# Kernel optimization log

Hardware: AMD Instinct MI355X
Metric: run time of the kernel (lower is better)

The kernel has to match this reference:

```python
import jax, jax.numpy as jnp
import numpy as np

B, S, Nv, D, DF, H = 8, 1024, 768, 512, 2048, 8
DH = D // H
EPS = 1e-5


def _layernorm(x, g, b):
    mu = jnp.mean(x, axis=-1, keepdims=True)
    var = jnp.mean((x - mu) ** 2, axis=-1, keepdims=True)
    return (x - mu) * jax.lax.rsqrt(var + EPS) * g + b


def _mha(x, Wq, Wk, Wv, Wo):
    b, s, d = x.shape
    q = (x @ Wq).reshape(b, s, H, DH)
    k = (x @ Wk).reshape(b, s, H, DH)
    v = (x @ Wv).reshape(b, s, H, DH)
    scores = jnp.einsum('bqhd,bkhd->bhqk', q, k) / np.sqrt(DH).astype(np.float32)
    a = jax.nn.softmax(scores, axis=-1)
    o = jnp.einsum('bhqk,bkhd->bqhd', a, v).reshape(b, s, d)
    return o @ Wo


def setup_inputs() -> dict:
    key = jax.random.key(0)
    ks = jax.random.split(key, 20)
    sc = 1.0 / np.sqrt(D)
    scf = 1.0 / np.sqrt(DF)
    n = lambda k, shp, s: (jax.random.normal(k, shp, jnp.float32) * s)
    return {
        'x': n(ks[0], (B, S, D), 1.0),
        'idx_emb_1': jax.random.randint(ks[1], (B, Nv), 0, Nv, dtype=jnp.int64) if jax.config.jax_enable_x64 else jax.random.randint(ks[1], (B, Nv), 0, Nv).astype(jnp.int32),
        'idx_pro_1': jax.random.randint(ks[2], (B, Nv), 0, Nv).astype(jnp.int32),
        'N': Nv,
        'Wq1': n(ks[3], (D, D), sc), 'Wk1': n(ks[4], (D, D), sc),
        'Wv1': n(ks[5], (D, D), sc), 'Wo1': n(ks[6], (D, D), sc),
        'Wq2': n(ks[7], (D, D), sc), 'Wk2': n(ks[8], (D, D), sc),
        'Wv2': n(ks[9], (D, D), sc), 'Wo2': n(ks[10], (D, D), sc),
        'w_conv1': n(ks[11], (D, DF), sc), 'b_conv1': jnp.zeros((DF,), jnp.float32),
        'w_conv2': n(ks[12], (DF, D), scf), 'b_conv2': jnp.zeros((D,), jnp.float32),
        'g1': jnp.ones((D,), jnp.float32), 'beta1': jnp.zeros((D,), jnp.float32),
        'g2': jnp.ones((D,), jnp.float32), 'beta2': jnp.zeros((D,), jnp.float32),
    }


def reference(x, idx_emb_1, idx_pro_1, N,
              Wq1, Wk1, Wv1, Wo1, Wq2, Wk2, Wv2, Wo2,
              w_conv1, b_conv1, w_conv2, b_conv2, g1, beta1, g2, beta2):
    # batched gather-reorder of first N tokens; rest pass through
    x_l1 = x.at[:, :N].set(jnp.take_along_axis(x[:, :N], idx_emb_1[:, :, None].astype(jnp.int32), axis=1))
    attn1 = _mha(x_l1, Wq1, Wk1, Wv1, Wo1)
    attn2 = jnp.flip(_mha(jnp.flip(x_l1, axis=1), Wq2, Wk2, Wv2, Wo2), axis=1)
    new_x1 = attn1 + attn2
    x_l2 = new_x1.at[:, :N].set(jnp.take_along_axis(new_x1[:, :N], idx_pro_1[:, :, None].astype(jnp.int32), axis=1))
    x = _layernorm(x + x_l2, g1, beta1)
    # kernel-size-1 Conv1d FFN == pointwise linear (dropout=0, eval mode)
    y = jnp.maximum(x @ w_conv1 + b_conv1, 0.0)
    y = y @ w_conv2 + b_conv2
    out = _layernorm(x + y, g2, beta2)
    return (out, attn1, attn2)
```

## Files before the change

kernel.cpp:

```cpp
#include <hip/hip_runtime.h>
#include <hip/hip_bf16.h>
#include <stdint.h>

#define B_ 8
#define S_ 1024
#define NV_ 768
#define D_ 512
#define DF_ 2048
#define H_ 8
#define DH_ 64
#define BS_ (B_*S_)
#define BSD_ ((size_t)B_*S_*D_)
#define QKLD 2048

typedef __bf16 bf16x8 __attribute__((ext_vector_type(8)));
typedef float f32x4 __attribute__((ext_vector_type(4)));
typedef float f32x16 __attribute__((ext_vector_type(16)));
typedef __hip_bfloat16 bf16;

__device__ __forceinline__ void async_copy16(const void* g, void* l) {
  __builtin_amdgcn_global_load_lds((const __attribute__((address_space(1))) void*)g,
                                   (__attribute__((address_space(3))) void*)l, 16, 0, 0);
}

__device__ __forceinline__ void stage_tile(const bf16* __restrict__ g, int gRow0, long ldg,
                                           int gCol0, bf16* lds, int rows, int tid) {
  const int totalBytes = rows << 7;
  for (int off = tid * 16; off < totalBytes; off += 4096) {
    const int r = off >> 7;
    const int c = off & 127;
    const int srcByte = c ^ ((r & 7) << 4);
    const bf16* gp = g + (long)(gRow0 + r) * ldg + gCol0 + (srcByte >> 1);
    async_copy16(gp, (char*)lds + off);
  }
}
__device__ __forceinline__ bf16x8 lds_frag(const bf16* base, int row, int kElem) {
  const int byte = (row << 7) + ((kElem << 1) ^ ((row & 7) << 4));
  return *(const bf16x8*)((const char*)base + byte);
}

__device__ __forceinline__ int fswz(int row) {
  return ((((row >> 3) & 3) << 1) | (row & 1)) << 4;
}

#define SCH_BIAS 1064872540.f
template<int BASE>
__device__ __forceinline__ bf16x8 pexp_frag(const f32x16& s) {
  union { unsigned u[4]; bf16x8 b; } r;
#pragma unroll
  for (int e = 0; e < 4; e++) {
    const int i0 = (int)fmaf(s[BASE + 2 * e], 8388608.f, SCH_BIAS);
    const int i1 = (int)fmaf(s[BASE + 2 * e + 1], 8388608.f, SCH_BIAS);
    r.u[e] = __builtin_amdgcn_perm((unsigned)i1, (unsigned)i0, 0x07060302u);
  }
  return r.b;
}

__device__ __forceinline__ bf16x8 ones_frag() {
  union { ushort u[8]; bf16x8 b; } r;
#pragma unroll
  for (int e = 0; e < 8; e++) r.u[e] = 0x3F80;
  return r.b;
}

__device__ __forceinline__ f32x16 zero16() {
  f32x16 z;
#pragma unroll
  for (int i = 0; i < 16; i++) z[i] = 0.f;
  return z;
}

struct WPanel { const float* src; bf16* dst; int srcLd, dstLd; float scale; };
struct WP16 { WPanel p[16]; };
__global__ __launch_bounds__(256) void wtrans16_kernel(WP16 ws) {
  __shared__ float tile[32][33];
  const WPanel pa = ws.p[blockIdx.z];
  const int tx = threadIdx.x, ty = threadIdx.y;
  const int n0 = blockIdx.x * 32, k0 = blockIdx.y * 32;
#pragma unroll
  for (int i = 0; i < 4; i++)
    tile[ty + i * 8][tx] = pa.src[(long)(k0 + ty + i * 8) * pa.srcLd + n0 + tx];
  __syncthreads();
#pragma unroll
  for (int i = 0; i < 4; i++)
    pa.dst[(long)(n0 + ty + i * 8) * pa.dstLd + k0 + tx] =
        __float2bfloat16(tile[tx][ty + i * 8] * pa.scale);
}

__global__ __launch_bounds__(256) void gather_cvt_kernel(const float* __restrict__ x,
                                                         const int* __restrict__ idx,
                                                         const int* __restrict__ Np,
                                                         bf16* __restrict__ out) {
  const int N = *Np;
  const int row = blockIdx.x * 2 + (threadIdx.x >> 7);
  const int t = threadIdx.x & 127;
  const int b = row >> 10, s = row & 1023;
  const int src = (s < N) ? idx[b * NV_ + s] : s;
  const float4 v = *(const float4*)(x + ((long)b * S_ + src) * D_ + t * 4);
  ushort4 u;
  u.x = (ushort)__bfloat16_as_ushort(__float2bfloat16(v.x));
  u.y = (ushort)__bfloat16_as_ushort(__float2bfloat16(v.y));
  u.z = (ushort)__bfloat16_as_ushort(__float2bfloat16(v.z));
  u.w = (ushort)__bfloat16_as_ushort(__float2bfloat16(v.w));
  *(ushort4*)(out + (long)row * D_ + t * 4) = u;
}

template<int BM, int BN, int MR, int NR, int OUTF, int BIAS, int RELU, int QKV>
__global__ __launch_bounds__(256) void gemm_bt(const bf16* __restrict__ A, long lda, long sAz,
                                               const bf16* __restrict__ Bt, long sBz,
                                               const float* __restrict__ bias,
                                               void* __restrict__ C, long ldc, long sCz,
                                               int K, bf16* __restrict__ vtbOut) {
  constexpr int WC = BN / (NR * 16);
  constexpr int WR = BM / (MR * 16);
  static_assert(WR * WC == 4, "4 waves");
  __shared__ bf16 As[BM * 64];
  __shared__ bf16 Bs[BN * 64];
  const int tid = threadIdx.x;
  const int lane = tid & 63, wave = tid >> 6;
  const int wr = wave / WC, wc = wave % WC;
  const int g = lane >> 4, lr = lane & 15;
  const int m0 = blockIdx.x * BM, n0 = blockIdx.y * BN;
  const int z = blockIdx.z;
  A += (long)z * sAz;
  Bt += (long)z * sBz;

  f32x4 acc[MR][NR];
#pragma unroll
  for (int m = 0; m < MR; m++)
#pragma unroll
    for (int n = 0; n < NR; n++) acc[m][n] = (f32x4){0.f, 0.f, 0.f, 0.f};

  for (int kt = 0; kt < K; kt += 64) {
    stage_tile(A, m0, lda, kt, As, BM, tid);
    stage_tile(Bt, n0, K, kt, Bs, BN, tid);
    __syncthreads();
#pragma unroll
    for (int ks = 0; ks < 64; ks += 32) {
      const int kk = ks + g * 8;
      bf16x8 aF[MR], bF[NR];
#pragma unroll
      for (int m = 0; m < MR; m++) aF[m] = lds_frag(As, wr * (MR * 16) + m * 16 + lr, kk);
#pragma unroll
      for (int n = 0; n < NR; n++) bF[n] = lds_frag(Bs, wc * (NR * 16) + n * 16 + lr, kk);
#pragma unroll
      for (int m = 0; m < MR; m++)
#pragma unroll
        for (int n = 0; n < NR; n++)
          acc[m][n] = __builtin_amdgcn_mfma_f32_16x16x32_bf16(aF[m], bF[n], acc[m][n], 0, 0, 0);
    }
    __syncthreads();
  }

#pragma unroll
  for (int m = 0; m < MR; m++) {
#pragma unroll
    for (int n = 0; n < NR; n++) {
      const int row = m0 + wr * (MR * 16) + m * 16 + g * 4;
      const int col = n0 + wc * (NR * 16) + n * 16 + lr;
      if (QKV) {
        const int set = (col >= 1536) ? 1 : 0;
        const int c1 = col - set * 1536;
        if (c1 < 1024) {
          bf16* cp = (bf16*)C + (long)row * QKLD + set * 1024 + c1;
#pragma unroll
          for (int r = 0; r < 4; r++) cp[(long)r * QKLD] = __float2bfloat16(acc[m][n][r]);
        } else {
          const int d = c1 - 1024;
          const int zz = set * 64 + ((row >> 10) << 3) + (d >> 6);
          const int s = row & 1023;
          const int sp = (s & ~12) | ((s & 4) << 1) | ((s & 8) >> 1);
          ushort4 pk;
          pk.x = (ushort)__bfloat16_as_ushort(__float2bfloat16(acc[m][n][0]));
          pk.y = (ushort)__bfloat16_as_ushort(__float2bfloat16(acc[m][n][1]));
          pk.z = (ushort)__bfloat16_as_ushort(__float2bfloat16(acc[m][n][2]));
          pk.w = (ushort)__bfloat16_as_ushort(__float2bfloat16(acc[m][n][3]));
          *(ushort4*)(vtbOut + (((long)(zz * 64 + (d & 63))) << 10) + sp) = pk;
        }
      } else {
        const float bv = BIAS ? bias[col] : 0.f;
#pragma unroll
        for (int r = 0; r < 4; r++) {
          float v = acc[m][n][r] + bv;
          if (RELU) v = fmaxf(v, 0.f);
          if (OUTF) ((float*)C)[(long)z * sCz + (long)(row + r) * ldc + col] = v;
          else ((bf16*)C)[(long)z * sCz + (long)(row + r) * ldc + col] = __float2bfloat16(v);
        }
      }
    }
  }
}

__global__ __launch_bounds__(256, 4) void flash_kernel(bf16* __restrict__ qk,
                                                       const bf16* __restrict__ vtb) {
  __shared__ char lds[32768];
  const int tid = threadIdx.x;
  const int lane = tid & 63, warp = tid >> 6;
  const int qlo = lane & 31, hi = lane >> 5;

  const int bid = (int)blockIdx.x;
  const int swz = (bid & 7) * 128 + (bid >> 3);
  const int qt = swz & 7;
  const int sbh = swz >> 3;
  const int set = sbh >> 6;
  const int b = (sbh >> 3) & 7, h = sbh & 7;

  bf16* Qp = qk + (long)b * S_ * QKLD + set * 1024 + h * DH_;
  const bf16* Kp = Qp + 512;
  const bf16* Vp = vtb + (long)sbh * DH_ * S_;

  const int r0 = tid >> 3;
  const int cbyt = (tid & 7) << 4;
  const int sb = cbyt ^ fswz(r0);
  char* const ld0 = lds + tid * 16;

  {
    const bf16* qS = Qp + (long)(qt * 128 + r0) * QKLD + (sb >> 1);
    async_copy16(qS, ld0);
    async_copy16(qS + 32 * QKLD, ld0 + 4096);
    async_copy16(qS + 64 * QKLD, ld0 + 8192);
    async_copy16(qS + 96 * QKLD, ld0 + 12288);
  }
  const bf16* kS = Kp + (long)r0 * QKLD + (sb >> 1);
  const bf16* vS = Vp + (long)r0 * S_ + (sb >> 1);
  async_copy16(kS, ld0 + 16384);
  async_copy16(kS + 32 * QKLD, ld0 + 16384 + 4096);
  async_copy16(vS, ld0 + 16384 + 8192);
  async_copy16(vS + 32 * S_, ld0 + 16384 + 12288);
  __syncthreads();

  const int qrow = warp * 32 + qlo;
  const int qrb = (qrow << 7) | fswz(qrow);
  bf16x8 qFh[4];
#pragma unroll
  for (int d4 = 0; d4 < 4; d4++)
    qFh[d4] = *(const bf16x8*)(lds + (qrb ^ (d4 * 32 + hi * 16)));
  __syncthreads();

  kS += 64 * QKLD; vS += 64;
  async_copy16(kS, ld0);
  async_copy16(kS + 32 * QKLD, ld0 + 4096);
  async_copy16(vS, ld0 + 8192);
  async_copy16(vS + 32 * S_, ld0 + 12288);

  f32x16 oAcc0 = zero16(), oAcc1 = zero16(), sAcc = zero16();
  const bf16x8 onesF = ones_frag();
  const int rb = (qlo << 7) | fswz(qlo);

  for (int t = 0; t < 16; t++) {
    const int bb = ((t & 1) ^ 1) << 14;
    const int kbase = bb + rb;
    const int vbase = bb + 8192 + rb;

    f32x16 s0 = zero16(), s1 = zero16();
    __builtin_amdgcn_s_setprio(1);
#pragma unroll
    for (int d4 = 0; d4 < 4; d4++) {
      const int kc2 = d4 * 32 + hi * 16;
      const bf16x8 kf0 = *(const bf16x8*)(lds + (kbase ^ kc2));
      const bf16x8 kf1 = *(const bf16x8*)(lds + ((kbase + 4096) ^ kc2));
      s0 = __builtin_amdgcn_mfma_f32_32x32x16_bf16(kf0, qFh[d4], s0, 0, 0, 0);
      s1 = __builtin_amdgcn_mfma_f32_32x32x16_bf16(kf1, qFh[d4], s1, 0, 0, 0);
    }
    __builtin_amdgcn_s_setprio(0);

    __builtin_amdgcn_s_setprio(1);
    {
      const bf16x8 pa0 = pexp_frag<0>(s0);
      oAcc0 = __builtin_amdgcn_mfma_f32_32x32x16_bf16(pa0, *(const bf16x8*)(lds + ((vbase) ^ (hi * 16))), oAcc0, 0, 0, 0);
      oAcc1 = __builtin_amdgcn_mfma_f32_32x32x16_bf16(pa0, *(const bf16x8*)(lds + ((vbase + 4096) ^ (hi * 16))), oAcc1, 0, 0, 0);
      sAcc = __builtin_amdgcn_mfma_f32_32x32x16_bf16(pa0, onesF, sAcc, 0, 0, 0);
      const bf16x8 pa1 = pexp_frag<8>(s0);
      oAcc0 = __builtin_amdgcn_mfma_f32_32x32x16_bf16(pa1, *(const bf16x8*)(lds + ((vbase) ^ (32 + hi * 16))), oAcc0, 0, 0, 0);
      oAcc1 = __builtin_amdgcn_mfma_f32_32x32x16_bf16(pa1, *(const bf16x8*)(lds + ((vbase + 4096) ^ (32 + hi * 16))), oAcc1, 0, 0, 0);
      sAcc = __builtin_amdgcn_mfma_f32_32x32x16_bf16(pa1, onesF, sAcc, 0, 0, 0);
      const bf16x8 pa2 = pexp_frag<0>(s1);
      oAcc0 = __builtin_amdgcn_mfma_f32_32x32x16_bf16(pa2, *(const bf16x8*)(lds + ((vbase) ^ (64 + hi * 16))), oAcc0, 0, 0, 0);
      oAcc1 = __builtin_amdgcn_mfma_f32_32x32x16_bf16(pa2, *(const bf16x8*)(lds + ((vbase + 4096) ^ (64 + hi * 16))), oAcc1, 0, 0, 0);
      sAcc = __builtin_amdgcn_mfma_f32_32x32x16_bf16(pa2, onesF, sAcc, 0, 0, 0);
      const bf16x8 pa3 = pexp_frag<8>(s1);
      oAcc0 = __builtin_amdgcn_mfma_f32_32x32x16_bf16(pa3, *(const bf16x8*)(lds + ((vbase) ^ (96 + hi * 16))), oAcc0, 0, 0, 0);
      oAcc1 = __builtin_amdgcn_mfma_f32_32x32x16_bf16(pa3, *(const bf16x8*)(lds + ((vbase + 4096) ^ (96 + hi * 16))), oAcc1, 0, 0, 0);
      sAcc = __builtin_amdgcn_mfma_f32_32x32x16_bf16(pa3, onesF, sAcc, 0, 0, 0);
    }
    __builtin_amdgcn_s_setprio(0);

    __syncthreads();
    if (t + 2 < 16) {
      kS += 64 * QKLD; vS += 64;
      char* dst = ld0 + bb;
      async_copy16(kS, dst);
      async_copy16(kS + 32 * QKLD, dst + 4096);
      async_copy16(vS, dst + 8192);
      async_copy16(vS + 32 * S_, dst + 12288);
    }
  }

#pragma unroll
  for (int r = 0; r < 16; r++) {
    const int q = (r & 3) + 8 * (r >> 2) + 4 * hi;
    const float linv = 1.f / sAcc[r];
    bf16* op = Qp + (long)(qt * 128 + warp * 32 + q) * QKLD;
    op[qlo] = __float2bfloat16(oAcc0[r] * linv);
    op[32 + qlo] = __float2bfloat16(oAcc1[r] * linv);
  }
}

__global__ __launch_bounds__(256) void fuse1_kernel(const float* __restrict__ x,
                                                    const float* __restrict__ a1,
                                                    const float* __restrict__ a2,
                                                    const int* __restrict__ idx,
                                                    const int* __restrict__ Np,
                                                    const float* __restrict__ gw,
                                                    const float* __restrict__ bw,
                                                    bf16* __restrict__ xlnB) {
  const int N = *Np;
  const int row = blockIdx.x * 4 + (threadIdx.x >> 6);
  const int lane = threadIdx.x & 63;
  const int b = row >> 10, s = row & 1023;
  const int j = (s < N) ? idx[b * NV_ + s] : s;
  const float* xp = x + (long)row * D_ + lane * 8;
  const float* p1 = a1 + ((long)b * S_ + j) * D_ + lane * 8;
  const float* p2 = a2 + ((long)b * S_ + j) * D_ + lane * 8;
  float v[8];
  float sum = 0.f;
#pragma unroll
  for (int q = 0; q < 2; q++) {
    const float4 t = ((const float4*)xp)[q];
    const float4 u = ((const float4*)p1)[q];
    const float4 w = ((const float4*)p2)[q];
    v[q * 4 + 0] = t.x + u.x + w.x; v[q * 4 + 1] = t.y + u.y + w.y;
    v[q * 4 + 2] = t.z + u.z + w.z; v[q * 4 + 3] = t.w + u.w + w.w;
  }
#pragma unroll
  for (int i = 0; i < 8; i++) sum += v[i];
#pragma unroll
  for (int o = 1; o < 64; o <<= 1) sum += __shfl_xor(sum, o, 64);
  const float mu = sum * (1.f / D_);
  float var = 0.f;
#pragma unroll
  for (int i = 0; i < 8; i++) { const float t = v[i] - mu; var += t * t; }
#pragma unroll
  for (int o = 1; o < 64; o <<= 1) var += __shfl_xor(var, o, 64);
  const float rs = rsqrtf(var * (1.f / D_) + 1e-5f);
#pragma unroll
  for (int i = 0; i < 8; i++) {
    const int d = lane * 8 + i;
    xlnB[(long)row * D_ + d] = __float2bfloat16((v[i] - mu) * rs * gw[d] + bw[d]);
  }
}

__global__ __launch_bounds__(256) void fuse2_kernel(const bf16* __restrict__ xlnB,
                                                    const bf16* __restrict__ ybf,
                                                    const float* __restrict__ gw,
                                                    const float* __restrict__ bw,
                                                    float* __restrict__ out) {
  const int row = blockIdx.x * 4 + (threadIdx.x >> 6);
  const int lane = threadIdx.x & 63;
  const bf16* xp = xlnB + (long)row * D_ + lane * 8;
  const bf16* yp = ybf + (long)row * D_ + lane * 8;
  float v[8];
  float sum = 0.f;
#pragma unroll
  for (int i = 0; i < 8; i++) {
    v[i] = __bfloat162float(xp[i]) + __bfloat162float(yp[i]);
    sum += v[i];
  }
#pragma unroll
  for (int o = 1; o < 64; o <<= 1) sum += __shfl_xor(sum, o, 64);
  const float mu = sum * (1.f / D_);
  float var = 0.f;
#pragma unroll
  for (int i = 0; i < 8; i++) { const float t = v[i] - mu; var += t * t; }
#pragma unroll
  for (int o = 1; o < 64; o <<= 1) var += __shfl_xor(var, o, 64);
  const float rs = rsqrtf(var * (1.f / D_) + 1e-5f);
#pragma unroll
  for (int i = 0; i < 8; i++) {
    const int d = lane * 8 + i;
    out[(long)row * D_ + d] = (v[i] - mu) * rs * gw[d] + bw[d];
  }
}

extern "C" void kernel_launch(void* const* d_in, const int* in_sizes, int n_in,
                              void* d_out, int out_size, void* d_ws, size_t ws_size,
                              hipStream_t stream) {
  const float* x   = (const float*)d_in[0];
  const int* idx1  = (const int*)d_in[1];
  const int* idx2  = (const int*)d_in[2];
  const int* Np    = (const int*)d_in[3];
  const float* b_conv1 = (const float*)d_in[13];
  const float* b_conv2 = (const float*)d_in[15];
  const float* g1    = (const float*)d_in[16];
  const float* beta1 = (const float*)d_in[17];
  const float* g2    = (const float*)d_in[18];
  const float* beta2 = (const float*)d_in[19];

  float* outp  = (float*)d_out;
  float* attn1 = outp + BSD_;

  const size_t DD = (size_t)D_ * D_;
  char* w = (char*)d_ws;
  bf16* wT  = (bf16*)w;
  bf16* w1T = wT + 8 * DD;
  bf16* w2T = w1T + (size_t)DF_ * D_;
  bf16* qk  = (bf16*)(w + (8ll << 20));
  bf16* xl1 = (bf16*)(w + (40ll << 20));
  bf16* xlnB = (bf16*)(w + (48ll << 20));
  bf16* vtb = (bf16*)(w + (56ll << 20));
  bf16* ffn = qk;
  bf16* ybf = xl1;

  WP16 wp;
  const float* attnW[8] = {(const float*)d_in[4], (const float*)d_in[5], (const float*)d_in[6],
                           (const float*)d_in[8], (const float*)d_in[9], (const float*)d_in[10],
                           (const float*)d_in[7], (const float*)d_in[11]};
  for (int z = 0; z < 8; z++) {
    wp.p[z].src = attnW[z];
    wp.p[z].dst = wT + (size_t)z * DD;
    wp.p[z].srcLd = D_; wp.p[z].dstLd = D_;
    wp.p[z].scale = (z == 0 || z == 3) ? 0.1803368801f : 1.f;
  }
  for (int j = 0; j < 4; j++) {
    wp.p[8 + j].src = (const float*)d_in[12] + 512 * j;
    wp.p[8 + j].dst = w1T + (size_t)(512 * j) * D_;
    wp.p[8 + j].srcLd = DF_; wp.p[8 + j].dstLd = D_;
    wp.p[8 + j].scale = 1.f;
  }
  for (int j = 0; j < 4; j++) {
    wp.p[12 + j].src = (const float*)d_in[14] + (size_t)(512 * j) * D_;
    wp.p[12 + j].dst = w2T + 512 * j;
    wp.p[12 + j].srcLd = D_; wp.p[12 + j].dstLd = DF_;
    wp.p[12 + j].scale = 1.f;
  }

  const dim3 tb(32, 8);
  wtrans16_kernel<<<dim3(16, 16, 16), tb, 0, stream>>>(wp);

  gather_cvt_kernel<<<BS_ / 2, 256, 0, stream>>>(x, idx1, Np, xl1);

  gemm_bt<128, 128, 4, 4, 0, 0, 0, 1><<<dim3(BS_ / 128, 3072 / 128, 1), 256, 0, stream>>>(
      xl1, D_, 0, wT, 0, nullptr, qk, QKLD, 0, D_, vtb);

  flash_kernel<<<1024, 256, 0, stream>>>(qk, vtb);

  gemm_bt<128, 128, 4, 4, 1, 0, 0, 0><<<dim3(BS_ / 128, D_ / 128, 2), 256, 0, stream>>>(
      qk, QKLD, 1024, wT + 6 * DD, (long)DD, nullptr, attn1, D_, (long)BSD_, D_, nullptr);

  fuse1_kernel<<<BS_ / 4, 256, 0, stream>>>(x, attn1, attn1 + BSD_, idx2, Np, g1, beta1, xlnB);

  gemm_bt<128, 128, 4, 4, 0, 1, 1, 0><<<dim3(BS_ / 128, DF_ / 128, 1), 256, 0, stream>>>(
      xlnB, D_, 0, w1T, 0, b_conv1, ffn, DF_, 0, D_, nullptr);
  gemm_bt<128, 64, 4, 2, 0, 1, 0, 0><<<dim3(BS_ / 128, D_ / 64, 1), 256, 0, stream>>>(
      ffn, DF_, 0, w2T, 0, b_conv2, ybf, D_, 0, DF_, nullptr);

  fuse2_kernel<<<BS_ / 4, 256, 0, stream>>>(xlnB, ybf, g2, beta2, outp);
}
```

Before: 193.8 us.

## Process two query sub-tiles per warp in flash attention to reuse K/V tiles

Each flash attention block now covers 256 query rows instead of 128, so every warp keeps two sets of Q fragments and accumulators and computes both against each K/V tile staged in LDS. The grid is halved and the block-index swizzle is updated to match. The aim is to halve K/V global loads and LDS fills per query and give the MFMA units more independent work per LDS read. The cost is higher register use, so launch bounds drop to 2 blocks per SM. With only 512 blocks, occupancy and latency hiding may suffer.

After: 186.8 us. 3.6% less time.

```diff
diff --git a/kernel.cpp b/kernel.cpp
--- a/kernel.cpp
+++ b/kernel.cpp
@@ -191,7 +191,7 @@
   }
 }
 
-__global__ __launch_bounds__(256, 4) void flash_kernel(bf16* __restrict__ qk,
+__global__ __launch_bounds__(256, 2) void flash_kernel(bf16* __restrict__ qk,
                                                        const bf16* __restrict__ vtb) {
   __shared__ char lds[32768];
   const int tid = threadIdx.x;
@@ -199,9 +199,9 @@
   const int qlo = lane & 31, hi = lane >> 5;
 
   const int bid = (int)blockIdx.x;
-  const int swz = (bid & 7) * 128 + (bid >> 3);
-  const int qt = swz & 7;
-  const int sbh = swz >> 3;
+  const int swz = (bid & 7) * 64 + (bid >> 3);
+  const int qt = swz & 3;
+  const int sbh = swz >> 2;
   const int set = sbh >> 6;
   const int b = (sbh >> 3) & 7, h = sbh & 7;
 
@@ -215,80 +215,83 @@
   char* const ld0 = lds + tid * 16;
 
   {
-    const bf16* qS = Qp + (long)(qt * 128 + r0) * QKLD + (sb >> 1);
-    async_copy16(qS, ld0);
-    async_copy16(qS + 32 * QKLD, ld0 + 4096);
-    async_copy16(qS + 64 * QKLD, ld0 + 8192);
-    async_copy16(qS + 96 * QKLD, ld0 + 12288);
-  }
+    const bf16* qS = Qp + (long)(qt * 256 + r0) * QKLD + (sb >> 1);
+#pragma unroll
+    for (int i = 0; i < 8; i++) async_copy16(qS + (long)i * 32 * QKLD, ld0 + i * 4096);
+  }
+  __syncthreads();
+
+  const int qrow = warp * 32 + qlo;
+  const int qrb = (qrow << 7) | fswz(qrow);
+  bf16x8 qA[4], qB[4];
+#pragma unroll
+  for (int d4 = 0; d4 < 4; d4++) {
+    const int kc2 = d4 * 32 + hi * 16;
+    qA[d4] = *(const bf16x8*)(lds + (qrb ^ kc2));
+    qB[d4] = *(const bf16x8*)(lds + ((qrb + 16384) ^ kc2));
+  }
+  __syncthreads();
+
   const bf16* kS = Kp + (long)r0 * QKLD + (sb >> 1);
   const bf16* vS = Vp + (long)r0 * S_ + (sb >> 1);
+  async_copy16(kS, ld0);
+  async_copy16(kS + 32 * QKLD, ld0 + 4096);
+  async_copy16(vS, ld0 + 8192);
+  async_copy16(vS + 32 * S_, ld0 + 12288);
+  __syncthreads();
+  kS += 64 * QKLD; vS += 64;
   async_copy16(kS, ld0 + 16384);
   async_copy16(kS + 32 * QKLD, ld0 + 16384 + 4096);
   async_copy16(vS, ld0 + 16384 + 8192);
   async_copy16(vS + 32 * S_, ld0 + 16384 + 12288);
-  __syncthreads();
-
-  const int qrow = warp * 32 + qlo;
-  const int qrb = (qrow << 7) | fswz(qrow);
-  bf16x8 qFh[4];
-#pragma unroll
-  for (int d4 = 0; d4 < 4; d4++)
-    qFh[d4] = *(const bf16x8*)(lds + (qrb ^ (d4 * 32 + hi * 16)));
-  __syncthreads();
-
-  kS += 64 * QKLD; vS += 64;
-  async_copy16(kS, ld0);
-  async_copy16(kS + 32 * QKLD, ld0 + 4096);
-  async_copy16(vS, ld0 + 8192);
-  async_copy16(vS + 32 * S_, ld0 + 12288);
-
-  f32x16 oAcc0 = zero16(), oAcc1 = zero16(), sAcc = zero16();
+
+  f32x16 oA0 = zero16(), oA1 = zero16(), sAccA = zero16();
+  f32x16 oB0 = zero16(), oB1 = zero16(), sAccB = zero16();
   const bf16x8 onesF = ones_frag();
   const int rb = (qlo << 7) | fswz(qlo);
 
+#pragma unroll 1
   for (int t = 0; t < 16; t++) {
-    const int bb = ((t & 1) ^ 1) << 14;
-    const int kbase = bb + rb;
-    const int vbase = bb + 8192 + rb;
-
-    f32x16 s0 = zero16(), s1 = zero16();
+    const int cbase = (t & 1) << 14;
+    const int kbase = cbase + rb;
+    const int vbase = cbase + 8192 + rb;
+
+    f32x16 sA0 = zero16(), sA1 = zero16(), sB0 = zero16(), sB1 = zero16();
     __builtin_amdgcn_s_setprio(1);
 #pragma unroll
     for (int d4 = 0; d4 < 4; d4++) {
       const int kc2 = d4 * 32 + hi * 16;
       const bf16x8 kf0 = *(const bf16x8*)(lds + (kbase ^ kc2));
       const bf16x8 kf1 = *(const bf16x8*)(lds + ((kbase + 4096) ^ kc2));
-      s0 = __builtin_amdgcn_mfma_f32_32x32x16_bf16(kf0, qFh[d4], s0, 0, 0, 0);
-      s1 = __builtin_amdgcn_mfma_f32_32x32x16_bf16(kf1, qFh[d4], s1, 0, 0, 0);
+      sA0 = __builtin_amdgcn_mfma_f32_32x32x16_bf16(kf0, qA[d4], sA0, 0, 0, 0);
+      sA1 = __builtin_amdgcn_mfma_f32_32x32x16_bf16(kf1, qA[d4], sA1, 0, 0, 0);
+      sB0 = __builtin_amdgcn_mfma_f32_32x32x16_bf16(kf0, qB[d4], sB0, 0, 0, 0);
+      sB1 = __builtin_amdgcn_mfma_f32_32x32x16_bf16(kf1, qB[d4], sB1, 0, 0, 0);
     }
-    __builtin_amdgcn_s_setprio(0);
-
-    __builtin_amdgcn_s_setprio(1);
-    {
-      const bf16x8 pa0 = pexp_frag<0>(s0);
-      oAcc0 = __builtin_amdgcn_mfma_f32_32x32x16_bf16(pa0, *(const bf16x8*)(lds + ((vbase) ^ (hi * 16))), oAcc0, 0, 0, 0);
-      oAcc1 = __builtin_amdgcn_mfma_f32_32x32x16_bf16(pa0, *(const bf16x8*)(lds + ((vbase + 4096) ^ (hi * 16))), oAcc1, 0, 0, 0);
-      sAcc = __builtin_amdgcn_mfma_f32_32x32x16_bf16(pa0, onesF, sAcc, 0, 0, 0);
-      const bf16x8 pa1 = pexp_frag<8>(s0);
-      oAcc0 = __builtin_amdgcn_mfma_f32_32x32x16_bf16(pa1, *(const bf16x8*)(lds + ((vbase) ^ (32 + hi * 16))), oAcc0, 0, 0, 0);
-      oAcc1 = __builtin_amdgcn_mfma_f32_32x32x16_bf16(pa1, *(const bf16x8*)(lds + ((vbase + 4096) ^ (32 + hi * 16))), oAcc1, 0, 0, 0);
-      sAcc = __builtin_amdgcn_mfma_f32_32x32x16_bf16(pa1, onesF, sAcc, 0, 0, 0);
-      const bf16x8 pa2 = pexp_frag<0>(s1);
-      oAcc0 = __builtin_amdgcn_mfma_f32_32x32x16_bf16(pa2, *(const bf16x8*)(lds + ((vbase) ^ (64 + hi * 16))), oAcc0, 0, 0, 0);
-      oAcc1 = __builtin_amdgcn_mfma_f32_32x32x16_bf16(pa2, *(const bf16x8*)(lds + ((vbase + 4096) ^ (64 + hi * 16))), oAcc1, 0, 0, 0);
-      sAcc = __builtin_amdgcn_mfma_f32_32x32x16_bf16(pa2, onesF, sAcc, 0, 0, 0);
-      const bf16x8 pa3 = pexp_frag<8>(s1);
-      oAcc0 = __builtin_amdgcn_mfma_f32_32x32x16_bf16(pa3, *(const bf16x8*)(lds + ((vbase) ^ (96 + hi * 16))), oAcc0, 0, 0, 0);
-      oAcc1 = __builtin_amdgcn_mfma_f32_32x32x16_bf16(pa3, *(const bf16x8*)(lds + ((vbase + 4096) ^ (96 + hi * 16))), oAcc1, 0, 0, 0);
-      sAcc = __builtin_amdgcn_mfma_f32_32x32x16_bf16(pa3, onesF, sAcc, 0, 0, 0);
+
+#pragma unroll
+    for (int ks = 0; ks < 4; ks++) {
+      bf16x8 paA, paB;
+      if (ks == 0)      { paA = pexp_frag<0>(sA0); paB = pexp_frag<0>(sB0); }
+      else if (ks == 1) { paA = pexp_frag<8>(sA0); paB = pexp_frag<8>(sB0); }
+      else if (ks == 2) { paA = pexp_frag<0>(sA1); paB = pexp_frag<0>(sB1); }
+      else              { paA = pexp_frag<8>(sA1); paB = pexp_frag<8>(sB1); }
+      const int off = ks * 32 + hi * 16;
+      const bf16x8 v0 = *(const bf16x8*)(lds + (vbase ^ off));
+      const bf16x8 v1 = *(const bf16x8*)(lds + ((vbase + 4096) ^ off));
+      oA0 = __builtin_amdgcn_mfma_f32_32x32x16_bf16(paA, v0, oA0, 0, 0, 0);
+      oA1 = __builtin_amdgcn_mfma_f32_32x32x16_bf16(paA, v1, oA1, 0, 0, 0);
+      sAccA = __builtin_amdgcn_mfma_f32_32x32x16_bf16(paA, onesF, sAccA, 0, 0, 0);
+      oB0 = __builtin_amdgcn_mfma_f32_32x32x16_bf16(paB, v0, oB0, 0, 0, 0);
+      oB1 = __builtin_amdgcn_mfma_f32_32x32x16_bf16(paB, v1, oB1, 0, 0, 0);
+      sAccB = __builtin_amdgcn_mfma_f32_32x32x16_bf16(paB, onesF, sAccB, 0, 0, 0);
     }
     __builtin_amdgcn_s_setprio(0);
 
     __syncthreads();
     if (t + 2 < 16) {
       kS += 64 * QKLD; vS += 64;
-      char* dst = ld0 + bb;
+      char* dst = ld0 + cbase;
       async_copy16(kS, dst);
       async_copy16(kS + 32 * QKLD, dst + 4096);
       async_copy16(vS, dst + 8192);
@@ -299,10 +302,14 @@
 #pragma unroll
   for (int r = 0; r < 16; r++) {
     const int q = (r & 3) + 8 * (r >> 2) + 4 * hi;
-    const float linv = 1.f / sAcc[r];
-    bf16* op = Qp + (long)(qt * 128 + warp * 32 + q) * QKLD;
-    op[qlo] = __float2bfloat16(oAcc0[r] * linv);
-    op[32 + qlo] = __float2bfloat16(oAcc1[r] * linv);
+    bf16* opA = Qp + (long)(qt * 256 + warp * 32 + q) * QKLD;
+    bf16* opB = opA + (long)128 * QKLD;
+    const float liA = 1.f / sAccA[r];
+    const float liB = 1.f / sAccB[r];
+    opA[qlo] = __float2bfloat16(oA0[r] * liA);
+    opA[32 + qlo] = __float2bfloat16(oA1[r] * liA);
+    opB[qlo] = __float2bfloat16(oB0[r] * liB);
+    opB[32 + qlo] = __float2bfloat16(oB1[r] * liB);
   }
 }
 
@@ -442,7 +449,7 @@
   gemm_bt<128, 128, 4, 4, 0, 0, 0, 1><<<dim3(BS_ / 128, 3072 / 128, 1), 256, 0, stream>>>(
       xl1, D_, 0, wT, 0, nullptr, qk, QKLD, 0, D_, vtb);
 
-  flash_kernel<<<1024, 256, 0, stream>>>(qk, vtb);
+  flash_kernel<<<512, 256, 0, stream>>>(qk, vtb);
 
   gemm_bt<128, 128, 4, 4, 1, 0, 0, 0><<<dim3(BS_ / 128, D_ / 128, 2), 256, 0, stream>>>(
       qk, QKLD, 1024, wT + 6 * DD, (long)DD, nullptr, attn1, D_, (long)BSD_, D_, nullptr);
```
